# Performance work log

Hardware: AMD Instinct MI355X
Metric: run time of the kernel (lower is better)

## Reference

```python
import jax, jax.numpy as jnp
import numpy as np

B, C, D = 32, 256, 768


def setup_inputs() -> dict:
    key = jax.random.key(0)
    k1, k2, k3, k4 = jax.random.split(key, 4)
    raw_features = jax.random.normal(k1, (B, D), dtype=jnp.float32)
    class_means = jax.random.normal(k2, (C, D), dtype=jnp.float32)
    # per-class normalized std diag (strictly positive divisor)
    class_diags = jax.random.uniform(k3, (C, D), dtype=jnp.float32) + 0.5
    # per-class inverse (shrunk, normalized) covariance; any dense matrix is
    # math-equivalent for the scoring kernel
    class_cov_invs = jax.random.normal(k4, (C, D, D), dtype=jnp.float32) * 0.01
    return {
        "raw_features": raw_features,
        "class_means": class_means,
        "class_diags": class_diags,
        "class_cov_invs": class_cov_invs,
    }


def reference(raw_features, class_means, class_diags, class_cov_invs):
    # Vectorized form of the per-class Python loop in compute_scores
    # (boundary_idx == 0 path; every class has stats, so no -1e9 fill).
    # x_norm[c] = x / diag_c ; mu_norm[c] = mean_c / diag_c
    diff = raw_features[None, :, :] / class_diags[:, None, :] \
        - (class_means / class_diags)[:, None, :]            # [C, B, D]
    temp = jnp.einsum('cbd,cde->cbe', diff, class_cov_invs)   # diff @ inv_c
    dist_sq = jnp.sum(temp * diff, axis=-1)                   # [C, B]
    scores_stack = -dist_sq.T                                 # [B, C]
    return scores_stack
```

## Files before the change

### kernel.cpp

```cpp
#include <hip/hip_runtime.h>
#include <hip/hip_bf16.h>


#define BATCH 32
#define NCLS 256
#define DIM 768
#define CHUNK 128
#define NCHUNK (DIM / CHUNK)
#define PADW (DIM + 8)

typedef __attribute__((ext_vector_type(8))) short bf16x8;
typedef __attribute__((ext_vector_type(4))) float f32x4;

__device__ __forceinline__ unsigned short f2bf(float f) {
    union { float f; unsigned u; } v; v.f = f;
    unsigned r = v.u + 0x7FFF + ((v.u >> 16) & 1);
    return (unsigned short)(r >> 16);
}
__device__ __forceinline__ float bf2f(unsigned short u) {
    union { unsigned u; float f; } v; v.u = ((unsigned)u) << 16;
    return v.f;
}

__global__ __launch_bounds__(256, 3) void fecam_kernel(
    const float* __restrict__ x,
    const float* __restrict__ means,
    const float* __restrict__ diags,
    const float* __restrict__ Minv,
    float* __restrict__ out)
{
    __shared__ unsigned short diff[BATCH][PADW];
    __shared__ float dist[BATCH];

    const int chunk = blockIdx.x;
    const int c     = blockIdx.y;
    const int tid   = threadIdx.x;

    if (tid < BATCH) dist[tid] = 0.f;

    for (int e = tid; e < DIM; e += 256) {
        float mv = means[c * DIM + e];
        float dv = diags[c * DIM + e];
        float rdv = 1.0f / dv;
        #pragma unroll 8
        for (int b = 0; b < BATCH; ++b) {
            diff[b][e] = f2bf((x[b * DIM + e] - mv) * rdv);
        }
    }
    __syncthreads();

    const int wave = tid >> 6;
    const int lane = tid & 63;
    const int l15  = lane & 15;
    const int quad = lane >> 4;

    const float* Mc = Minv + (size_t)c * DIM * DIM;

    for (int t = 0; t < 2; ++t) {
        const int d0 = chunk * CHUNK + (wave * 2 + t) * 16;
        const float* rowp = Mc + (size_t)(d0 + l15) * DIM + quad * 8;

        f32x4 acc0 = {0.f, 0.f, 0.f, 0.f};
        f32x4 acc1 = {0.f, 0.f, 0.f, 0.f};

        float4 la = *(const float4*)(rowp);
        float4 lb = *(const float4*)(rowp + 4);

        for (int kb = 0; kb < DIM; kb += 32) {
            bf16x8 afrag;
            afrag[0] = (short)f2bf(la.x); afrag[1] = (short)f2bf(la.y);
            afrag[2] = (short)f2bf(la.z); afrag[3] = (short)f2bf(la.w);
            afrag[4] = (short)f2bf(lb.x); afrag[5] = (short)f2bf(lb.y);
            afrag[6] = (short)f2bf(lb.z); afrag[7] = (short)f2bf(lb.w);

            if (kb + 32 < DIM) {
                rowp += 32;
                la = *(const float4*)(rowp);
                lb = *(const float4*)(rowp + 4);
            }

            bf16x8 b0 = *(const bf16x8*)&diff[l15][kb + quad * 8];
            bf16x8 b1 = *(const bf16x8*)&diff[16 + l15][kb + quad * 8];

            acc0 = __builtin_amdgcn_mfma_f32_16x16x32_bf16(afrag, b0, acc0, 0, 0, 0);
            acc1 = __builtin_amdgcn_mfma_f32_16x16x32_bf16(afrag, b1, acc1, 0, 0, 0);
        }

        #pragma unroll
        for (int nt = 0; nt < 2; ++nt) {
            f32x4 acc = nt ? acc1 : acc0;
            const int b = nt * 16 + l15;
            float s = 0.f;
            #pragma unroll
            for (int r = 0; r < 4; ++r) {
                const int d = d0 + quad * 4 + r;
                s += acc[r] * bf2f(diff[b][d]);
            }
            s += __shfl_xor(s, 16);
            s += __shfl_xor(s, 32);
            if (lane < 16) atomicAdd(&dist[b], s);
        }
    }

    __syncthreads();
    if (tid < BATCH) atomicAdd(&out[tid * NCLS + c], -dist[tid]);
}

extern "C" void kernel_launch(void* const* d_in, const int* in_sizes, int n_in,
                              void* d_out, int out_size, void* d_ws, size_t ws_size,
                              hipStream_t stream) {
    const float* x     = (const float*)d_in[0];
    const float* means = (const float*)d_in[1];
    const float* diags = (const float*)d_in[2];
    const float* Minv  = (const float*)d_in[3];
    float* out = (float*)d_out;

    hipMemsetAsync(out, 0, (size_t)BATCH * NCLS * sizeof(float), stream);

    dim3 grid(NCHUNK, NCLS);
    fecam_kernel<<<grid, 256, 0, stream>>>(x, means, diags, Minv, out);
}
```

Baseline: 764.3 us.

## Double row tiles per wave with two-stage nontemporal prefetch and larger chunks

```diff
diff --git a/kernel.cpp b/kernel.cpp
--- a/kernel.cpp
+++ b/kernel.cpp
@@ -5,8 +5,9 @@
 #define BATCH 32
 #define NCLS 256
 #define DIM 768
-#define CHUNK 128
+#define CHUNK 256
 #define NCHUNK (DIM / CHUNK)
+#define NTHREADS 512
 #define PADW (DIM + 8)
 
 typedef __attribute__((ext_vector_type(8))) short bf16x8;
@@ -21,8 +22,17 @@
     union { unsigned u; float f; } v; v.u = ((unsigned)u) << 16;
     return v.f;
 }
+__device__ __forceinline__ f32x4 ntload(const float* p) {
+    return __builtin_nontemporal_load((const f32x4*)p);
+}
+__device__ __forceinline__ void cvt8(const f32x4& a, const f32x4& b, bf16x8& o) {
+    o[0] = (short)f2bf(a[0]); o[1] = (short)f2bf(a[1]);
+    o[2] = (short)f2bf(a[2]); o[3] = (short)f2bf(a[3]);
+    o[4] = (short)f2bf(b[0]); o[5] = (short)f2bf(b[1]);
+    o[6] = (short)f2bf(b[2]); o[7] = (short)f2bf(b[3]);
+}
 
-__global__ __launch_bounds__(256, 3) void fecam_kernel(
+__global__ __launch_bounds__(NTHREADS, 4) void fecam_kernel(
     const float* __restrict__ x,
     const float* __restrict__ means,
     const float* __restrict__ diags,
@@ -38,14 +48,12 @@
 
     if (tid < BATCH) dist[tid] = 0.f;
 
-    for (int e = tid; e < DIM; e += 256) {
-        float mv = means[c * DIM + e];
-        float dv = diags[c * DIM + e];
-        float rdv = 1.0f / dv;
+    for (int e = tid; e < DIM; e += NTHREADS) {
+        float mv  = means[c * DIM + e];
+        float rdv = 1.0f / diags[c * DIM + e];
         #pragma unroll 8
-        for (int b = 0; b < BATCH; ++b) {
+        for (int b = 0; b < BATCH; ++b)
             diff[b][e] = f2bf((x[b * DIM + e] - mv) * rdv);
-        }
     }
     __syncthreads();
 
@@ -54,52 +62,63 @@
     const int l15  = lane & 15;
     const int quad = lane >> 4;
 
-    const float* Mc = Minv + (size_t)c * DIM * DIM;
+    const int d0 = chunk * CHUNK + wave * 32;
+    const float* row0 = Minv + (size_t)c * DIM * DIM + (size_t)(d0 + l15) * DIM + quad * 8;
+    const float* row1 = row0 + 16 * DIM;
 
-    for (int t = 0; t < 2; ++t) {
-        const int d0 = chunk * CHUNK + (wave * 2 + t) * 16;
-        const float* rowp = Mc + (size_t)(d0 + l15) * DIM + quad * 8;
+    f32x4 acc00 = {0.f,0.f,0.f,0.f};
+    f32x4 acc01 = {0.f,0.f,0.f,0.f};
+    f32x4 acc10 = {0.f,0.f,0.f,0.f};
+    f32x4 acc11 = {0.f,0.f,0.f,0.f};
 
-        f32x4 acc0 = {0.f, 0.f, 0.f, 0.f};
-        f32x4 acc1 = {0.f, 0.f, 0.f, 0.f};
+    f32x4 pf[2][4];
+    pf[0][0] = ntload(row0);      pf[0][1] = ntload(row0 + 4);
+    pf[0][2] = ntload(row1);      pf[0][3] = ntload(row1 + 4);
+    pf[1][0] = ntload(row0 + 32); pf[1][1] = ntload(row0 + 36);
+    pf[1][2] = ntload(row1 + 32); pf[1][3] = ntload(row1 + 36);
 
-        float4 la = *(const float4*)(rowp);
-        float4 lb = *(const float4*)(rowp + 4);
+#define KSTEP(S, KB)                                                          \
+    {                                                                         \
+        bf16x8 a0, a1;                                                        \
+        cvt8(pf[S][0], pf[S][1], a0);                                         \
+        cvt8(pf[S][2], pf[S][3], a1);                                         \
+        if ((KB) + 64 < DIM) {                                                \
+            pf[S][0] = ntload(row0 + (KB) + 64);                              \
+            pf[S][1] = ntload(row0 + (KB) + 68);                              \
+            pf[S][2] = ntload(row1 + (KB) + 64);                              \
+            pf[S][3] = ntload(row1 + (KB) + 68);                              \
+        }                                                                     \
+                 \
+        bf16x8 b0 = *(const bf16x8*)&diff[l15][(KB) + quad * 8];              \
+        bf16x8 b1 = *(const bf16x8*)&diff[16 + l15][(KB) + quad * 8];         \
+        acc00 = __builtin_amdgcn_mfma_f32_16x16x32_bf16(a0, b0, acc00, 0,0,0);\
+        acc01 = __builtin_amdgcn_mfma_f32_16x16x32_bf16(a0, b1, acc01, 0,0,0);\
+        acc10 = __builtin_amdgcn_mfma_f32_16x16x32_bf16(a1, b0, acc10, 0,0,0);\
+        acc11 = __builtin_amdgcn_mfma_f32_16x16x32_bf16(a1, b1, acc11, 0,0,0);\
+    }
 
-        for (int kb = 0; kb < DIM; kb += 32) {
-            bf16x8 afrag;
-            afrag[0] = (short)f2bf(la.x); afrag[1] = (short)f2bf(la.y);
-            afrag[2] = (short)f2bf(la.z); afrag[3] = (short)f2bf(la.w);
-            afrag[4] = (short)f2bf(lb.x); afrag[5] = (short)f2bf(lb.y);
-            afrag[6] = (short)f2bf(lb.z); afrag[7] = (short)f2bf(lb.w);
+    #pragma unroll
+    for (int kb = 0; kb < DIM; kb += 64) {
+        KSTEP(0, kb);
+        KSTEP(1, kb + 32);
+    }
+#undef KSTEP
 
-            if (kb + 32 < DIM) {
-                rowp += 32;
-                la = *(const float4*)(rowp);
-                lb = *(const float4*)(rowp + 4);
-            }
-
-            bf16x8 b0 = *(const bf16x8*)&diff[l15][kb + quad * 8];
-            bf16x8 b1 = *(const bf16x8*)&diff[16 + l15][kb + quad * 8];
-
-            acc0 = __builtin_amdgcn_mfma_f32_16x16x32_bf16(afrag, b0, acc0, 0, 0, 0);
-            acc1 = __builtin_amdgcn_mfma_f32_16x16x32_bf16(afrag, b1, acc1, 0, 0, 0);
-        }
-
-        #pragma unroll
-        for (int nt = 0; nt < 2; ++nt) {
-            f32x4 acc = nt ? acc1 : acc0;
-            const int b = nt * 16 + l15;
-            float s = 0.f;
-            #pragma unroll
-            for (int r = 0; r < 4; ++r) {
-                const int d = d0 + quad * 4 + r;
-                s += acc[r] * bf2f(diff[b][d]);
-            }
-            s += __shfl_xor(s, 16);
-            s += __shfl_xor(s, 32);
-            if (lane < 16) atomicAdd(&dist[b], s);
-        }
+    float s0 = 0.f, s1 = 0.f;
+    #pragma unroll
+    for (int r = 0; r < 4; ++r) {
+        const int dA = d0 + quad * 4 + r;
+        const int dB = dA + 16;
+        s0 += acc00[r] * bf2f(diff[l15][dA]);
+        s0 += acc10[r] * bf2f(diff[l15][dB]);
+        s1 += acc01[r] * bf2f(diff[16 + l15][dA]);
+        s1 += acc11[r] * bf2f(diff[16 + l15][dB]);
+    }
+    s0 += __shfl_xor(s0, 16); s0 += __shfl_xor(s0, 32);
+    s1 += __shfl_xor(s1, 16); s1 += __shfl_xor(s1, 32);
+    if (lane < 16) {
+        atomicAdd(&dist[l15], s0);
+        atomicAdd(&dist[16 + l15], s1);
     }
 
     __syncthreads();
@@ -115,8 +134,8 @@
     const float* Minv  = (const float*)d_in[3];
     float* out = (float*)d_out;
 
-    hipMemsetAsync(out, 0, (size_t)BATCH * NCLS * sizeof(float), stream);
+    (void)hipMemsetAsync(out, 0, (size_t)BATCH * NCLS * sizeof(float), stream);
 
     dim3 grid(NCHUNK, NCLS);
-    fecam_kernel<<<grid, 256, 0, stream>>>(x, means, diags, Minv, out);
+    fecam_kernel<<<grid, NTHREADS, 0, stream>>>(x, means, diags, Minv, out);
 }
```

After: 760.6 us. About the same (-0.5%).
